# Performance work log

Measured on AMD Instinct MI355X. Metric: run time of the kernel, lower is better.

The kernel has to match this reference:

```python
import jax, jax.numpy as jnp
import numpy as np
from jax import lax

PAD = 2       # kernel_size=5 -> pad=2
DT = 0.1
NLAYERS = 3

def _circ_pad(x, p=PAD):
    # F.pad(..., mode='circular') on H,W
    return jnp.pad(x, ((0, 0), (0, 0), (p, p), (p, p)), mode='wrap')

def _conv(x, w):
    # torch Conv2d semantics (cross-correlation), NCHW/OIHW, valid padding
    return lax.conv_general_dilated(x, w, (1, 1), 'VALID',
                                    dimension_numbers=('NCHW', 'OIHW', 'NCHW'))

def _gradient(U, K1_w, K2_w):
    # k1 = relu(K1(U)) with circular padding: [B,2,H,W]
    k1 = jax.nn.relu(_conv(_circ_pad(U), K1_w))
    # lam = K2.weight * k1, K2_w shape (1,2,1,1) broadcasts over B,H,W
    lam = K2_w * k1
    # conv_transpose2d(circ_pad(lam), K1_w, padding=4, stride=1)
    # == valid conv with channel-swapped, spatially flipped kernel (k-1-4 = 0 extra pad)
    wT = jnp.transpose(jnp.flip(K1_w, (2, 3)), (1, 0, 2, 3))  # (1,2,5,5)
    return _conv(_circ_pad(lam), wT)  # [B,1,H,W]

def setup_inputs() -> dict:
    key = jax.random.key(0)
    kU, k1, kA = jax.random.split(key, 3)
    B, H, W = 16, 1024, 1024
    U = jax.random.normal(kU, (B, 1, H, W), jnp.float32)
    K1_w = jax.random.normal(k1, (2, 1, 5, 5), jnp.float32) * 0.2
    K2_w = jnp.ones((1, 2, 1, 1), jnp.float32)  # source sets K2 weight to ones
    A_w = jax.random.normal(kA, (1, 1, 5, 5), jnp.float32) * 0.2
    return {"U": U, "K1_w": K1_w, "K2_w": K2_w, "A_w": A_w}

def reference(U, K1_w, K2_w, A_w):
    # explicit Euler: U <- U + dt/nlayers * A(gradient(U)), repeated nlayers times
    for _ in range(NLAYERS):
        grad = _gradient(U, K1_w, K2_w)
        vec = _conv(_circ_pad(grad), A_w)  # self.A (circular conv 1->1)
        U = U + (DT / NLAYERS) * vec
    return U
```

## Files before the change

kernel.cpp:

```cpp
#include <hip/hip_runtime.h>

#define HH 1024
#define WW 1024
#define TW 32
#define TH 64
#define SUS 44
#define SLS 44
#define SGS 36
#define DTC (0.1f/3.0f)


__global__ __launch_bounds__(256, 4) void pde_layer(
    const float* __restrict__ Uin,
    const float* __restrict__ K1,
    const float* __restrict__ K2,
    const float* __restrict__ Aw,
    float* __restrict__ Uout)
{
    __shared__ __align__(16) float sUG[76 * SUS];
    __shared__ __align__(16) float sL0[72 * SLS];
    __shared__ __align__(16) float sL1[72 * SLS];
    float* const sU = sUG;
    float* const sG = sUG;

    const int tid = threadIdx.x;
    const int bx = blockIdx.x * TW;
    const int by = blockIdx.y * TH;
    const size_t plane = (size_t)blockIdx.z * (size_t)(HH * WW);
    const float* __restrict__ Ub = Uin + plane;
    float* __restrict__ Ob = Uout + plane;

    float w0[25], w1[25], aw[25];
    #pragma unroll
    for (int t = 0; t < 25; ++t) { w0[t] = K1[t]; w1[t] = K1[25 + t]; aw[t] = Aw[t]; }
    const float k2a = K2[0], k2b = K2[1];

    const bool xedge = (bx == 0) || (bx + TW == WW);
    if (!xedge) {
        for (int it = tid; it < 76 * 11; it += 256) {
            int r = it / 11;
            int q = it - r * 11;
            int gr = (by + r - 6) & (HH - 1);
            const float* row = Ub + ((size_t)gr << 10);
            int c = bx - 6 + (q << 2);
            float2 a = *(const float2*)(row + c);
            float2 b = *(const float2*)(row + c + 2);
            float4 v; v.x = a.x; v.y = a.y; v.z = b.x; v.w = b.y;
            *(float4*)&sU[r * SUS + (q << 2)] = v;
        }
    } else {
        for (int it = tid; it < 76 * 11; it += 256) {
            int r = it / 11;
            int q = it - r * 11;
            int gr = (by + r - 6) & (HH - 1);
            const float* row = Ub + ((size_t)gr << 10);
            int c = bx - 6 + (q << 2);
            float4 v;
            v.x = row[(c + 0) & (WW - 1)];
            v.y = row[(c + 1) & (WW - 1)];
            v.z = row[(c + 2) & (WW - 1)];
            v.w = row[(c + 3) & (WW - 1)];
            *(float4*)&sU[r * SUS + (q << 2)] = v;
        }
    }
    __syncthreads();

    if (tid < 180) {
        const int rg = tid / 10;
        const int cg = tid - rg * 10;
        const float* src = &sU[(rg * 4) * SUS + cg * 4];
        float acc0[4][4] = {}, acc1[4][4] = {};
        #pragma unroll
        for (int ri = 0; ri < 8; ++ri) {
            float u[8];
            *(float4*)&u[0] = *(const float4*)&src[ri * SUS];
            *(float4*)&u[4] = *(const float4*)&src[ri * SUS + 4];
            #pragma unroll
            for (int k = 0; k < 4; ++k) {
                const int i = ri - k;
                if (i >= 0 && i < 5) {
                    #pragma unroll
                    for (int j = 0; j < 5; ++j) {
                        const float a = w0[i * 5 + j];
                        const float b = w1[i * 5 + j];
                        #pragma unroll
                        for (int cq = 0; cq < 4; ++cq) {
                            acc0[k][cq] = fmaf(u[cq + j], a, acc0[k][cq]);
                            acc1[k][cq] = fmaf(u[cq + j], b, acc1[k][cq]);
                        }
                    }
                }
            }
        }
        #pragma unroll
        for (int k = 0; k < 4; ++k) {
            float4 o0, o1;
            o0.x = fmaxf(acc0[k][0], 0.f) * k2a;  o1.x = fmaxf(acc1[k][0], 0.f) * k2b;
            o0.y = fmaxf(acc0[k][1], 0.f) * k2a;  o1.y = fmaxf(acc1[k][1], 0.f) * k2b;
            o0.z = fmaxf(acc0[k][2], 0.f) * k2a;  o1.z = fmaxf(acc1[k][2], 0.f) * k2b;
            o0.w = fmaxf(acc0[k][3], 0.f) * k2a;  o1.w = fmaxf(acc1[k][3], 0.f) * k2b;
            *(float4*)&sL0[(rg * 4 + k) * SLS + cg * 4] = o0;
            *(float4*)&sL1[(rg * 4 + k) * SLS + cg * 4] = o1;
        }
    }
    __syncthreads();

    if (tid < 153) {
        const int rg = tid / 9;
        const int cg = tid - rg * 9;
        const float* p0 = &sL0[(rg * 4) * SLS + cg * 4];
        const float* p1 = &sL1[(rg * 4) * SLS + cg * 4];
        float acc[4][4] = {};
        #pragma unroll
        for (int ri = 0; ri < 8; ++ri) {
            float u0[8], u1[8];
            *(float4*)&u0[0] = *(const float4*)&p0[ri * SLS];
            *(float4*)&u0[4] = *(const float4*)&p0[ri * SLS + 4];
            *(float4*)&u1[0] = *(const float4*)&p1[ri * SLS];
            *(float4*)&u1[4] = *(const float4*)&p1[ri * SLS + 4];
            #pragma unroll
            for (int k = 0; k < 4; ++k) {
                const int i = ri - k;
                if (i >= 0 && i < 5) {
                    #pragma unroll
                    for (int j = 0; j < 5; ++j) {
                        const float a = w0[24 - (i * 5 + j)];
                        const float b = w1[24 - (i * 5 + j)];
                        #pragma unroll
                        for (int cq = 0; cq < 4; ++cq) {
                            acc[k][cq] = fmaf(u0[cq + j], a, acc[k][cq]);
                            acc[k][cq] = fmaf(u1[cq + j], b, acc[k][cq]);
                        }
                    }
                }
            }
        }
        #pragma unroll
        for (int k = 0; k < 4; ++k) {
            float4 o; o.x = acc[k][0]; o.y = acc[k][1]; o.z = acc[k][2]; o.w = acc[k][3];
            *(float4*)&sG[(rg * 4 + k) * SGS + cg * 4] = o;
        }
    }
    __syncthreads();

    if (tid < 128) {
        const int rg = tid >> 3;
        const int cg = tid & 7;
        const float* p = &sG[(rg * 4) * SGS + cg * 4];
        float acc[4][4] = {};
        #pragma unroll
        for (int ri = 0; ri < 8; ++ri) {
            float u[8];
            *(float4*)&u[0] = *(const float4*)&p[ri * SGS];
            *(float4*)&u[4] = *(const float4*)&p[ri * SGS + 4];
            #pragma unroll
            for (int k = 0; k < 4; ++k) {
                const int i = ri - k;
                if (i >= 0 && i < 5) {
                    #pragma unroll
                    for (int j = 0; j < 5; ++j) {
                        const float a = aw[i * 5 + j];
                        #pragma unroll
                        for (int cq = 0; cq < 4; ++cq)
                            acc[k][cq] = fmaf(u[cq + j], a, acc[k][cq]);
                    }
                }
            }
        }
        #pragma unroll
        for (int k = 0; k < 4; ++k) {
            const int gy = by + rg * 4 + k;
            const int gx = bx + cg * 4;
            float4 id = *(const float4*)&Ub[((size_t)gy << 10) + gx];
            float4 o;
            o.x = id.x + DTC * acc[k][0];
            o.y = id.y + DTC * acc[k][1];
            o.z = id.z + DTC * acc[k][2];
            o.w = id.w + DTC * acc[k][3];
            *(float4*)&Ob[((size_t)gy << 10) + gx] = o;
        }
    }
}

extern "C" void kernel_launch(void* const* d_in, const int* in_sizes, int n_in,
                              void* d_out, int out_size, void* d_ws, size_t ws_size,
                              hipStream_t stream) {
    const float* U  = (const float*)d_in[0];
    const float* K1 = (const float*)d_in[1];
    const float* K2 = (const float*)d_in[2];
    const float* Aw = (const float*)d_in[3];
    float* out = (float*)d_out;
    float* ws  = (float*)d_ws;

    const int B = in_sizes[0] / (HH * WW);
    dim3 grid(WW / TW, HH / TH, B);

    pde_layer<<<grid, 256, 0, stream>>>(U,   K1, K2, Aw, out);
    pde_layer<<<grid, 256, 0, stream>>>(out, K1, K2, Aw, ws);
    pde_layer<<<grid, 256, 0, stream>>>(ws,  K1, K2, Aw, out);
}
```

Before: 282.2 us.

## Use wide tiles, single shared lambda buffer, and read residual from shared

Changes the tile from 32x64 to 64x32 and shrinks shared memory by reusing one buffer for both lambda channels in turn. The second channel stays in registers while the first is consumed, which adds two extra barriers. The launch-bounds occupancy hint rises from 4 to 6 blocks. The residual add now reads U from the shared tile instead of global memory. Risks include register pressure from keeping acc1 live across phases and the cost of the extra syncs.

```diff
diff --git a/kernel.cpp b/kernel.cpp
--- a/kernel.cpp
+++ b/kernel.cpp
@@ -2,26 +2,24 @@
 
 #define HH 1024
 #define WW 1024
-#define TW 32
-#define TH 64
-#define SUS 44
-#define SLS 44
-#define SGS 36
+#define TW 64
+#define TH 32
+#define SUS 76
+#define SLS 76
+#define SGS 68
 #define DTC (0.1f/3.0f)
 
-
-__global__ __launch_bounds__(256, 4) void pde_layer(
+__global__ __launch_bounds__(256, 6) void pde_layer(
     const float* __restrict__ Uin,
     const float* __restrict__ K1,
     const float* __restrict__ K2,
     const float* __restrict__ Aw,
     float* __restrict__ Uout)
 {
-    __shared__ __align__(16) float sUG[76 * SUS];
-    __shared__ __align__(16) float sL0[72 * SLS];
-    __shared__ __align__(16) float sL1[72 * SLS];
-    float* const sU = sUG;
-    float* const sG = sUG;
+    __shared__ __align__(16) float sU[44 * SUS];
+    __shared__ __align__(16) float sLG[40 * SLS];
+    float* const sL = sLG;
+    float* const sG = sLG;
 
     const int tid = threadIdx.x;
     const int bx = blockIdx.x * TW;
@@ -37,9 +35,8 @@
 
     const bool xedge = (bx == 0) || (bx + TW == WW);
     if (!xedge) {
-        for (int it = tid; it < 76 * 11; it += 256) {
-            int r = it / 11;
-            int q = it - r * 11;
+        for (int it = tid; it < 44 * 19; it += 256) {
+            int r = it / 19, q = it - r * 19;
             int gr = (by + r - 6) & (HH - 1);
             const float* row = Ub + ((size_t)gr << 10);
             int c = bx - 6 + (q << 2);
@@ -49,9 +46,8 @@
             *(float4*)&sU[r * SUS + (q << 2)] = v;
         }
     } else {
-        for (int it = tid; it < 76 * 11; it += 256) {
-            int r = it / 11;
-            int q = it - r * 11;
+        for (int it = tid; it < 44 * 19; it += 256) {
+            int r = it / 19, q = it - r * 19;
             int gr = (by + r - 6) & (HH - 1);
             const float* row = Ub + ((size_t)gr << 10);
             int c = bx - 6 + (q << 2);
@@ -65,11 +61,21 @@
     }
     __syncthreads();
 
-    if (tid < 180) {
-        const int rg = tid / 10;
-        const int cg = tid - rg * 10;
-        const float* src = &sU[(rg * 4) * SUS + cg * 4];
-        float acc0[4][4] = {}, acc1[4][4] = {};
+    float acc1[4][4];
+    float gacc[4][4];
+
+    const int rg1 = tid / 18, cg1 = tid - (tid / 18) * 18;
+    const int rg2 = tid / 17, cg2 = tid - (tid / 17) * 17;
+    const bool s1 = (tid < 180);
+    const bool s2 = (tid < 153);
+
+    if (s1) {
+        const float* src = &sU[(rg1 * 4) * SUS + cg1 * 4];
+        float acc0[4][4] = {};
+        #pragma unroll
+        for (int k = 0; k < 4; ++k)
+            #pragma unroll
+            for (int c = 0; c < 4; ++c) acc1[k][c] = 0.f;
         #pragma unroll
         for (int ri = 0; ri < 8; ++ri) {
             float u[8];
@@ -94,30 +100,27 @@
         }
         #pragma unroll
         for (int k = 0; k < 4; ++k) {
-            float4 o0, o1;
-            o0.x = fmaxf(acc0[k][0], 0.f) * k2a;  o1.x = fmaxf(acc1[k][0], 0.f) * k2b;
-            o0.y = fmaxf(acc0[k][1], 0.f) * k2a;  o1.y = fmaxf(acc1[k][1], 0.f) * k2b;
-            o0.z = fmaxf(acc0[k][2], 0.f) * k2a;  o1.z = fmaxf(acc1[k][2], 0.f) * k2b;
-            o0.w = fmaxf(acc0[k][3], 0.f) * k2a;  o1.w = fmaxf(acc1[k][3], 0.f) * k2b;
-            *(float4*)&sL0[(rg * 4 + k) * SLS + cg * 4] = o0;
-            *(float4*)&sL1[(rg * 4 + k) * SLS + cg * 4] = o1;
-        }
-    }
-    __syncthreads();
-
-    if (tid < 153) {
-        const int rg = tid / 9;
-        const int cg = tid - rg * 9;
-        const float* p0 = &sL0[(rg * 4) * SLS + cg * 4];
-        const float* p1 = &sL1[(rg * 4) * SLS + cg * 4];
-        float acc[4][4] = {};
-        #pragma unroll
-        for (int ri = 0; ri < 8; ++ri) {
-            float u0[8], u1[8];
-            *(float4*)&u0[0] = *(const float4*)&p0[ri * SLS];
-            *(float4*)&u0[4] = *(const float4*)&p0[ri * SLS + 4];
-            *(float4*)&u1[0] = *(const float4*)&p1[ri * SLS];
-            *(float4*)&u1[4] = *(const float4*)&p1[ri * SLS + 4];
+            float4 o;
+            o.x = fmaxf(acc0[k][0], 0.f) * k2a;
+            o.y = fmaxf(acc0[k][1], 0.f) * k2a;
+            o.z = fmaxf(acc0[k][2], 0.f) * k2a;
+            o.w = fmaxf(acc0[k][3], 0.f) * k2a;
+            *(float4*)&sL[(rg1 * 4 + k) * SLS + cg1 * 4] = o;
+        }
+    }
+    __syncthreads();
+
+    if (s2) {
+        #pragma unroll
+        for (int k = 0; k < 4; ++k)
+            #pragma unroll
+            for (int c = 0; c < 4; ++c) gacc[k][c] = 0.f;
+        const float* p = &sL[(rg2 * 4) * SLS + cg2 * 4];
+        #pragma unroll
+        for (int ri = 0; ri < 8; ++ri) {
+            float u[8];
+            *(float4*)&u[0] = *(const float4*)&p[ri * SLS];
+            *(float4*)&u[4] = *(const float4*)&p[ri * SLS + 4];
             #pragma unroll
             for (int k = 0; k < 4; ++k) {
                 const int i = ri - k;
@@ -125,27 +128,65 @@
                     #pragma unroll
                     for (int j = 0; j < 5; ++j) {
                         const float a = w0[24 - (i * 5 + j)];
-                        const float b = w1[24 - (i * 5 + j)];
-                        #pragma unroll
-                        for (int cq = 0; cq < 4; ++cq) {
-                            acc[k][cq] = fmaf(u0[cq + j], a, acc[k][cq]);
-                            acc[k][cq] = fmaf(u1[cq + j], b, acc[k][cq]);
-                        }
-                    }
-                }
-            }
-        }
-        #pragma unroll
-        for (int k = 0; k < 4; ++k) {
-            float4 o; o.x = acc[k][0]; o.y = acc[k][1]; o.z = acc[k][2]; o.w = acc[k][3];
-            *(float4*)&sG[(rg * 4 + k) * SGS + cg * 4] = o;
+                        #pragma unroll
+                        for (int cq = 0; cq < 4; ++cq)
+                            gacc[k][cq] = fmaf(u[cq + j], a, gacc[k][cq]);
+                    }
+                }
+            }
+        }
+    }
+    __syncthreads();
+
+    if (s1) {
+        #pragma unroll
+        for (int k = 0; k < 4; ++k) {
+            float4 o;
+            o.x = fmaxf(acc1[k][0], 0.f) * k2b;
+            o.y = fmaxf(acc1[k][1], 0.f) * k2b;
+            o.z = fmaxf(acc1[k][2], 0.f) * k2b;
+            o.w = fmaxf(acc1[k][3], 0.f) * k2b;
+            *(float4*)&sL[(rg1 * 4 + k) * SLS + cg1 * 4] = o;
+        }
+    }
+    __syncthreads();
+
+    if (s2) {
+        const float* p = &sL[(rg2 * 4) * SLS + cg2 * 4];
+        #pragma unroll
+        for (int ri = 0; ri < 8; ++ri) {
+            float u[8];
+            *(float4*)&u[0] = *(const float4*)&p[ri * SLS];
+            *(float4*)&u[4] = *(const float4*)&p[ri * SLS + 4];
+            #pragma unroll
+            for (int k = 0; k < 4; ++k) {
+                const int i = ri - k;
+                if (i >= 0 && i < 5) {
+                    #pragma unroll
+                    for (int j = 0; j < 5; ++j) {
+                        const float a = w1[24 - (i * 5 + j)];
+                        #pragma unroll
+                        for (int cq = 0; cq < 4; ++cq)
+                            gacc[k][cq] = fmaf(u[cq + j], a, gacc[k][cq]);
+                    }
+                }
+            }
+        }
+    }
+    __syncthreads();
+
+    if (s2) {
+        #pragma unroll
+        for (int k = 0; k < 4; ++k) {
+            float4 o; o.x = gacc[k][0]; o.y = gacc[k][1]; o.z = gacc[k][2]; o.w = gacc[k][3];
+            *(float4*)&sG[(rg2 * 4 + k) * SGS + cg2 * 4] = o;
         }
     }
     __syncthreads();
 
     if (tid < 128) {
-        const int rg = tid >> 3;
-        const int cg = tid & 7;
+        const int rg = tid >> 4;
+        const int cg = tid & 15;
         const float* p = &sG[(rg * 4) * SGS + cg * 4];
         float acc[4][4] = {};
         #pragma unroll
@@ -169,15 +210,15 @@
         }
         #pragma unroll
         for (int k = 0; k < 4; ++k) {
-            const int gy = by + rg * 4 + k;
-            const int gx = bx + cg * 4;
-            float4 id = *(const float4*)&Ub[((size_t)gy << 10) + gx];
+            const int r = rg * 4 + k;
+            float2 i0 = *(const float2*)&sU[(r + 6) * SUS + cg * 4 + 6];
+            float2 i1 = *(const float2*)&sU[(r + 6) * SUS + cg * 4 + 8];
             float4 o;
-            o.x = id.x + DTC * acc[k][0];
-            o.y = id.y + DTC * acc[k][1];
-            o.z = id.z + DTC * acc[k][2];
-            o.w = id.w + DTC * acc[k][3];
-            *(float4*)&Ob[((size_t)gy << 10) + gx] = o;
+            o.x = i0.x + DTC * acc[k][0];
+            o.y = i0.y + DTC * acc[k][1];
+            o.z = i1.x + DTC * acc[k][2];
+            o.w = i1.y + DTC * acc[k][3];
+            *(float4*)&Ob[((size_t)(by + r) << 10) + bx + cg * 4] = o;
         }
     }
 }
```

Result: faster. 269.2 us (-4.6%).
